# Kernel optimization log

Measured on AMD Instinct MI355X. Metric: run time of the kernel, lower is better.

The kernel has to match this reference:

```python
import jax, jax.numpy as jnp
import numpy as np

N, E, H, ED = 50000, 400000, 512, 64
BN_EPS = 1e-5


def setup_inputs() -> dict:
    key = jax.random.key(0)
    ks = jax.random.split(key, 8)
    s = lambda d: 1.0 / np.sqrt(d)
    return {
        "x": jax.random.normal(ks[0], (N, H), jnp.float32),
        "edge_attr": jax.random.normal(ks[1], (E, ED), jnp.float32),
        "edge_index": jax.random.randint(ks[2], (2, E), 0, N, jnp.int32),
        # GINEConv edge projection (edge_dim -> hidden_dim)
        "W_e": jax.random.normal(ks[3], (ED, H), jnp.float32) * s(ED),
        "b_e": jnp.zeros((H,), jnp.float32),
        # 2-layer MLP: Linear(H, 2H) -> BN -> SiLU -> Linear(2H, H)
        "W1": jax.random.normal(ks[4], (H, 2 * H), jnp.float32) * s(H),
        "b1": jnp.zeros((2 * H,), jnp.float32),
        "g1": jnp.ones((2 * H,), jnp.float32),
        "beta1": jnp.zeros((2 * H,), jnp.float32),
        "W2": jax.random.normal(ks[5], (2 * H, H), jnp.float32) * s(2 * H),
        "b2": jnp.zeros((H,), jnp.float32),
        # outer BatchNorm(hidden_dim)
        "g2": jnp.ones((H,), jnp.float32),
        "beta2": jnp.zeros((H,), jnp.float32),
        # trainable GIN epsilon (init 0)
        "eps": jnp.zeros((), jnp.float32),
    }


def _bn(h, g, b):
    # training-mode batch norm over the node dimension (biased variance)
    mu = jnp.mean(h, axis=0)
    var = jnp.mean(jnp.square(h - mu), axis=0)
    return (h - mu) * jax.lax.rsqrt(var + BN_EPS) * g + b


def reference(x, edge_attr, edge_index, W_e, b_e, W1, b1, g1, beta1, W2, b2, g2, beta2, eps):
    src, dst = edge_index[0], edge_index[1]
    # message: ReLU(x_j + lin(e_ij)), gathered per edge  -> [E, H]
    msg = jax.nn.relu(x[src] + edge_attr @ W_e + b_e)
    # scatter-add aggregate into destination nodes -> [N, H]
    aggr = jax.ops.segment_sum(msg, dst, num_segments=x.shape[0])
    # GIN combine + 2-layer MLP with internal BatchNorm + SiLU (dropout=0)
    h = (1.0 + eps) * x + aggr
    h = jax.nn.silu(_bn(h @ W1 + b1, g1, beta1))
    h = h @ W2 + b2
    # outer BatchNorm + SiLU (dropout=0 -> identity)
    return jax.nn.silu(_bn(h, g2, beta2))
```

## Files before the change

### kernel.cpp

```cpp
#include <hip/hip_runtime.h>
#include <math.h>

#define NN 50000
#define NE 400000
#define HD 512
#define EDIM 64
#define H2 1024
#define LDT 72
#define CAP_SLOT 1200000
#define CAP_TILE 75000
#define CAP_HEAVY 8192
#define NBLK_SCAN 98

typedef short s16x8 __attribute__((ext_vector_type(8)));
typedef float f32x4 __attribute__((ext_vector_type(4)));

__device__ __forceinline__ unsigned short f2bf(float f) {
    union { float f; unsigned u; } v; v.f = f;
    unsigned r = v.u + 0x7fffu + ((v.u >> 16) & 1u);
    return (unsigned short)(r >> 16);
}
__device__ __forceinline__ float bf2f(unsigned short h) {
    union { unsigned u; float f; } v; v.u = ((unsigned)h) << 16;
    return v.f;
}
__device__ __forceinline__ float silu_f(float t) {
    return t / (1.f + __expf(-t));
}
__device__ __forceinline__ void gload_lds16(const unsigned short* g, unsigned short* l) {
    __builtin_amdgcn_global_load_lds(
        (const __attribute__((address_space(1))) unsigned int*)(g),
        (__attribute__((address_space(3))) unsigned int*)(l), 16, 0, 0);
}

constexpr size_t OFF_AGGRC = 0;
constexpr size_t OFF_XB   = 16777216;
constexpr size_t OFF_H1   = 0;
constexpr size_t OFF_H    = 102400000;
constexpr size_t OFF_WET  = 153600000;
constexpr size_t OFF_W1T  = OFF_WET + 65536;
constexpr size_t OFF_W2T  = OFF_W1T + 1048576;
constexpr size_t OFF_CNT  = OFF_W2T + 1048576;
constexpr size_t OFF_B1S  = OFF_CNT + 200000;
constexpr size_t OFF_B1Q  = OFF_B1S + 4096;
constexpr size_t OFF_B2S  = OFF_B1Q + 4096;
constexpr size_t OFF_B2Q  = OFF_B2S + 2048;
constexpr size_t ZERO_BYTES = 200000 + 4096 + 4096 + 2048 + 2048;
constexpr size_t OFF_TEX  = OFF_B2Q + 2048;
constexpr size_t OFF_BSUM = OFF_TEX + 200000;
constexpr size_t OFF_BOFF = OFF_BSUM + 512;
constexpr size_t OFF_T    = OFF_BOFF + 512;
constexpr size_t OFF_CUR  = OFF_T + 64;
constexpr size_t OFF_NOT  = OFF_CUR + 200000;
constexpr size_t OFF_SRCP = OFF_NOT + 300032;
constexpr size_t OFF_EIXP = OFF_SRCP + 4800000;
constexpr size_t OFF_SC1  = OFF_EIXP + 4800000;
constexpr size_t OFF_SB1  = OFF_SC1 + 4096;
constexpr size_t OFF_SC2  = OFF_SB1 + 4096;
constexpr size_t OFF_SB2  = OFF_SC2 + 2048;

__global__ __launch_bounds__(256) void k_convert(const float* __restrict__ We,
    const float* __restrict__ W1, const float* __restrict__ W2,
    unsigned short* __restrict__ wet, unsigned short* __restrict__ w1t,
    unsigned short* __restrict__ w2t) {
    int i = blockIdx.x * 256 + threadIdx.x;
    if (i < 32768) {
        int n = i >> 6, k = i & 63;
        wet[i] = f2bf(We[k * HD + n]);
    } else if (i < 32768 + 524288) {
        int j = i - 32768;
        int n = j >> 9, k = j & 511;
        w1t[j] = f2bf(W1[k * H2 + n]);
    } else if (i < 32768 + 2 * 524288) {
        int j = i - (32768 + 524288);
        int n = j >> 10, k = j & 1023;
        w2t[j] = f2bf(W2[k * HD + n]);
    }
}

__global__ __launch_bounds__(256) void k_xconv(const float* __restrict__ x,
    unsigned short* __restrict__ xb) {
    int t = blockIdx.x * 256 + threadIdx.x;
    if (t >= NN * 64) return;
    int n = t >> 6, rem = t & 63;
    int cb = rem >> 4, l = rem & 15;
    const float* src = x + (size_t)n * HD + cb * 128 + l;
    unsigned short o[8];
    #pragma unroll
    for (int j = 0; j < 8; ++j) o[j] = f2bf(src[j * 16]);
    *(uint4*)(xb + (size_t)n * HD + cb * 128 + l * 8) = *(const uint4*)o;
}

__global__ __launch_bounds__(256) void k_hist(const int* __restrict__ dst, int* __restrict__ counts) {
    int e = blockIdx.x * 256 + threadIdx.x;
    if (e < NE) atomicAdd(&counts[dst[e]], 1);
}

__global__ __launch_bounds__(512) void k_scan1(const int* __restrict__ counts,
    int* __restrict__ tile_excl, int* __restrict__ bsum) {
    __shared__ int wsums[8];
    int b = blockIdx.x, t = threadIdx.x;
    int i = b * 512 + t;
    int c = (i < NN) ? counts[i] : 0;
    int v = 0;
    if (c > 8) v = (c + 15) >> 4;
    else if (c >= 1) v = 0x10000;
    int lane = t & 63, wid = t >> 6;
    int x = v;
    #pragma unroll
    for (int o = 1; o < 64; o <<= 1) {
        int y = __shfl_up(x, o, 64);
        if (lane >= o) x += y;
    }
    if (lane == 63) wsums[wid] = x;
    __syncthreads();
    if (t == 0) {
        int run = 0;
        for (int w = 0; w < 8; ++w) { int tmp = wsums[w]; wsums[w] = run; run += tmp; }
    }
    __syncthreads();
    int excl = x - v + wsums[wid];
    if (i < NN) tile_excl[i] = excl;
    if (t == 511) bsum[b] = excl + v;
}

__global__ void k_scan2(int* __restrict__ bsum, int* __restrict__ boff, int* __restrict__ Tout) {
    if (threadIdx.x == 0) {
        int runf = 0, runh = 0;
        for (int b = 0; b < NBLK_SCAN; ++b) {
            int pk = bsum[b];
            boff[b] = runf;
            bsum[b] = runh;
            runf += pk & 0xFFFF;
            runh += pk >> 16;
        }
        Tout[0] = runf;
        Tout[1] = 0;
        Tout[2] = runh;
    }
}

__global__ __launch_bounds__(512) void k_scan3(const int* __restrict__ counts,
    int* __restrict__ tile_excl, const int* __restrict__ boff, const int* __restrict__ bsum,
    int* __restrict__ cursor, int* __restrict__ node_of_tile, int* __restrict__ Tout) {
    int b = blockIdx.x, t = threadIdx.x;
    int i = b * 512 + t;
    if (i >= NN) return;
    int c = counts[i];
    int pk = tile_excl[i];
    int hid = -1;
    if (c >= 1 && c <= 8) {
        int halfidx = (pk >> 16) + bsum[b];
        int tile = Tout[0] + (halfidx >> 1);
        cursor[i] = tile * 16 + (halfidx & 1) * 8;
        ((unsigned short*)node_of_tile)[tile * 2 + (halfidx & 1)] = (unsigned short)i;
    } else if (c > 8) {
        int tc = (c + 15) >> 4;
        int ts = (pk & 0xFFFF) + boff[b];
        cursor[i] = ts * 16;
        if (c <= 16) {
            node_of_tile[ts] = (int)(0xFFFF0000u | (unsigned)i);
        } else {
            hid = atomicAdd(&Tout[1], 1);
            if (hid >= CAP_HEAVY) hid = CAP_HEAVY - 1;
            for (int k = 0; k < tc; ++k)
                node_of_tile[ts + k] = (int)(0xFFFE0000u | (unsigned)hid);
        }
    }
    tile_excl[i] = hid;
}

__global__ __launch_bounds__(256) void k_scatter(const int* __restrict__ src, const int* __restrict__ dst,
    int* __restrict__ cursor, int* __restrict__ srcp, int* __restrict__ eidxp) {
    int e = blockIdx.x * 256 + threadIdx.x;
    if (e < NE) {
        int d = dst[e];
        int p = atomicAdd(&cursor[d], 1);
        srcp[p] = src[e];
        eidxp[p] = e;
    }
}

__global__ __launch_bounds__(256, 4) void k_edge(
    const float* __restrict__ ea, const unsigned short* __restrict__ wet,
    const unsigned short* __restrict__ xb, const float* __restrict__ b_e,
    const float* __restrict__ eps,
    const int* __restrict__ srcp, const int* __restrict__ eidxp,
    const int* __restrict__ node_of_tile, const int* __restrict__ Tptr,
    float* __restrict__ aggrc, unsigned short* __restrict__ h) {
    int tile0 = blockIdx.x * 2;
    int T = Tptr[0] + ((Tptr[2] + 1) >> 1);
    if (tile0 >= T) return;
    __shared__ unsigned short As[32 * LDT];
    __shared__ int Ss[32];
    __shared__ float Rs[4][256];
    int t = threadIdx.x;
    int slot0 = tile0 * 16;
    {
        int r = t >> 3, qq = t & 7;
        int s = srcp[slot0 + r];
        if (qq == 0) Ss[r] = s;
        unsigned short* lp = As + r * LDT + qq * 8;
        if (s >= 0) {
            int eix = eidxp[slot0 + r];
            const float* gp = ea + (size_t)eix * EDIM + qq * 8;
            float4 v0 = ((const float4*)gp)[0];
            float4 v1 = ((const float4*)gp)[1];
            lp[0] = f2bf(v0.x); lp[1] = f2bf(v0.y); lp[2] = f2bf(v0.z); lp[3] = f2bf(v0.w);
            lp[4] = f2bf(v1.x); lp[5] = f2bf(v1.y); lp[6] = f2bf(v1.z); lp[7] = f2bf(v1.w);
        } else {
            uint4 z = {0u, 0u, 0u, 0u};
            *(uint4*)lp = z;
        }
    }
    __syncthreads();
    int wave = t >> 6, lane = t & 63, l15 = lane & 15, quad = lane >> 4;
    int cblk = wave * 128;
    f32x4 acc[2][8];
    #pragma unroll
    for (int i = 0; i < 2; ++i)
        #pragma unroll
        for (int j = 0; j < 8; ++j) acc[i][j] = (f32x4){0.f, 0.f, 0.f, 0.f};
    #pragma unroll
    for (int k0 = 0; k0 < 64; k0 += 32) {
        s16x8 af[2], bfr[8];
        #pragma unroll
        for (int i = 0; i < 2; ++i)
            af[i] = *(const s16x8*)(As + (i * 16 + l15) * LDT + k0 + quad * 8);
        #pragma unroll
        for (int j = 0; j < 8; ++j)
            bfr[j] = *(const s16x8*)(wet + (size_t)(cblk + j * 16 + l15) * EDIM + k0 + quad * 8);
        #pragma unroll
        for (int i = 0; i < 2; ++i)
            #pragma unroll
            for (int j = 0; j < 8; ++j)
                acc[i][j] = __builtin_amdgcn_mfma_f32_16x16x32_bf16(af[i], bfr[j], acc[i][j], 0, 0, 0);
    }
    float ep = 1.0f + eps[0];
    float bev[8];
    #pragma unroll
    for (int j = 0; j < 8; ++j) bev[j] = b_e[cblk + j * 16 + l15];
    float* rp = Rs[wave];
    #pragma unroll
    for (int i = 0; i < 2; ++i) {
        int tile = tile0 + i;
        unsigned meta = (unsigned)node_of_tile[tile];
        unsigned idA = meta & 0xFFFFu, idB = meta >> 16;
        bool pair = idB < 0xFFFEu;
        int v_own = pair ? (quad < 2 ? (int)idA : (int)idB) : (int)idA;
        int vc = v_own < NN ? v_own : 0;
        int srow = i * 16 + quad * 4;
        s16x8 xr[4]; float msk[4];
        #pragma unroll
        for (int r = 0; r < 4; ++r) {
            int s = Ss[srow + r];
            msk[r] = s >= 0 ? 1.f : 0.f;
            xr[r] = *(const s16x8*)(xb + (size_t)(s >= 0 ? s : 0) * HD + cblk + l15 * 8);
        }
        s16x8 xo = *(const s16x8*)(xb + (size_t)vc * HD + cblk + l15 * 8);
        float sum8[8];
        #pragma unroll
        for (int j = 0; j < 8; ++j) sum8[j] = 0.f;
        #pragma unroll
        for (int r = 0; r < 4; ++r) {
            #pragma unroll
            for (int j = 0; j < 8; ++j) {
                float vv = acc[i][j][r] + bf2f((unsigned short)xr[r][j]) + bev[j];
                vv = vv > 0.f ? vv : 0.f;
                sum8[j] = fmaf(msk[r], vv, sum8[j]);
            }
        }
        #pragma unroll
        for (int j = 0; j < 8; ++j) sum8[j] += __shfl_xor(sum8[j], 16, 64);
        if (tile < T) {
            if (pair) {
                #pragma unroll
                for (int j = 0; j < 8; ++j) {
                    float val = fmaf(ep, bf2f((unsigned short)xo[j]), sum8[j]);
                    if (quad == 0) rp[j * 16 + l15] = val;
                    if (quad == 2) rp[128 + j * 16 + l15] = val;
                }
                __builtin_amdgcn_sched_barrier(0);
                int l2 = lane & 31;
                const float* rb_ = rp + (lane >> 5) * 128 + l2 * 4;
                float4 v4 = *(const float4*)rb_;
                uint2 pk;
                pk.x = (unsigned)f2bf(v4.x) | ((unsigned)f2bf(v4.y) << 16);
                pk.y = (unsigned)f2bf(v4.z) | ((unsigned)f2bf(v4.w) << 16);
                *(uint2*)(h + (size_t)v_own * HD + cblk + l2 * 4) = pk;
            } else {
                #pragma unroll
                for (int j = 0; j < 8; ++j) sum8[j] += __shfl_xor(sum8[j], 32, 64);
                if (idB == 0xFFFEu) {
                    if (quad == 0) {
                        float* ap = aggrc + (size_t)idA * HD + cblk;
                        #pragma unroll
                        for (int j = 0; j < 8; ++j) atomicAdd(ap + j * 16 + l15, sum8[j]);
                    }
                } else {
                    int j0 = quad * 2, j1 = j0 + 1;
                    rp[j0 * 16 + l15] = fmaf(ep, bf2f((unsigned short)xo[j0]), sum8[j0]);
                    rp[j1 * 16 + l15] = fmaf(ep, bf2f((unsigned short)xo[j1]), sum8[j1]);
                    __builtin_amdgcn_sched_barrier(0);
                    unsigned pk = (unsigned)f2bf(rp[lane * 2]) |
                                  ((unsigned)f2bf(rp[lane * 2 + 1]) << 16);
                    *(unsigned*)(h + (size_t)idA * HD + cblk + lane * 2) = pk;
                }
            }
        }
    }
}

__global__ __launch_bounds__(256) void k_combine_heavy(const float* __restrict__ aggrc,
    const float* __restrict__ x, const int* __restrict__ counts, const int* __restrict__ hidmap,
    const float* __restrict__ eps, unsigned short* __restrict__ h) {
    long i = ((long)blockIdx.x * 256 + threadIdx.x) * 4;
    if (i >= (long)NN * HD) return;
    int v = (int)(i >> 9);
    int c = counts[v];
    if (c >= 1 && c <= 16) return;
    float ep = 1.0f + eps[0];
    float4 a = {0.f, 0.f, 0.f, 0.f};
    if (c > 16) a = *(const float4*)(aggrc + (size_t)hidmap[v] * HD + (i & (HD - 1)));
    float4 xv = *(const float4*)(x + i);
    uint2 p;
    p.x = (unsigned)f2bf(ep * xv.x + a.x) | ((unsigned)f2bf(ep * xv.y + a.y) << 16);
    p.y = (unsigned)f2bf(ep * xv.z + a.z) | ((unsigned)f2bf(ep * xv.w + a.w) << 16);
    *(uint2*)(h + i) = p;
}

template <bool BF16OUT, bool SILU_A>
__global__ __launch_bounds__(256) void k_gemm_bn(
    const unsigned short* __restrict__ A, const unsigned short* __restrict__ Bt,
    const float* __restrict__ bias, void* __restrict__ Cv,
    float* __restrict__ bn_sum, float* __restrict__ bn_sumsq,
    const float* __restrict__ a_sc, const float* __restrict__ a_sb,
    int M, int K, int Nn) {
    __shared__ unsigned short As[SILU_A ? (64 * LDT) : (64 * 64)];
    __shared__ unsigned short Bs[128 * 64];
    __shared__ float csum[128], csumsq[128];
    constexpr int LDA = SILU_A ? LDT : 64;
    int nwg = gridDim.x;
    int q = nwg >> 3, r = nwg & 7;
    int xk = blockIdx.x & 7, xj = blockIdx.x >> 3;
    int logical = xk * q + (xk < r ? xk : r) + xj;
    int nnb = Nn >> 7;
    int mblk = logical / nnb, nblk = logical - mblk * nnb;
    int t = threadIdx.x;
    int row0 = mblk * 64, col0 = nblk * 128;
    int wid = t >> 6, lane = t & 63, l15 = lane & 15, quad = lane >> 4;
    int wr = wid >> 1, wc = wid & 1;
    int rb = (lane >> 3), cb8 = (lane & 7) * 8;
    int scb8 = cb8 ^ (rb * 8);
    int rswz = (l15 & 7) * 8;
    f32x4 acc[2][4];
    #pragma unroll
    for (int i = 0; i < 2; ++i)
        #pragma unroll
        for (int j = 0; j < 4; ++j) acc[i][j] = (f32x4){0.f, 0.f, 0.f, 0.f};

    for (int k0 = 0; k0 < K; k0 += 64) {
        __syncthreads();
        #pragma unroll
        for (int c = 0; c < 4; ++c) {
            int row = (wid * 4 + c) * 8 + rb;
            gload_lds16(Bt + (size_t)(col0 + row) * K + k0 + scb8,
                        Bs + row * 64 + cb8);
        }
        if constexpr (!SILU_A) {
            #pragma unroll
            for (int c = 0; c < 2; ++c) {
                int row = (wid * 2 + c) * 8 + rb;
                gload_lds16(A + (size_t)(row0 + row) * K + k0 + scb8,
                            As + row * 64 + cb8);
            }
        } else {
            int rr = t >> 2, qtr = t & 3;
            int row = row0 + rr;
            int kb = k0 + qtr * 16;
            unsigned short* lp = As + rr * LDT + qtr * 16;
            if (row < M) {
                const unsigned short* gp = A + (size_t)row * K + kb;
                #pragma unroll
                for (int jj = 0; jj < 2; ++jj) {
                    uint4 u = *(const uint4*)(gp + jj * 8);
                    float4 sA = *(const float4*)(a_sc + kb + jj * 8);
                    float4 sB = *(const float4*)(a_sc + kb + jj * 8 + 4);
                    float4 bA = *(const float4*)(a_sb + kb + jj * 8);
                    float4 bB = *(const float4*)(a_sb + kb + jj * 8 + 4);
                    unsigned short o[8];
                    o[0] = f2bf(silu_f(bf2f((unsigned short)(u.x & 0xffffu)) * sA.x + bA.x));
                    o[1] = f2bf(silu_f(bf2f((unsigned short)(u.x >> 16)) * sA.y + bA.y));
                    o[2] = f2bf(silu_f(bf2f((unsigned short)(u.y & 0xffffu)) * sA.z + bA.z));
                    o[3] = f2bf(silu_f(bf2f((unsigned short)(u.y >> 16)) * sA.w + bA.w));
                    o[4] = f2bf(silu_f(bf2f((unsigned short)(u.z & 0xffffu)) * sB.x + bB.x));
                    o[5] = f2bf(silu_f(bf2f((unsigned short)(u.z >> 16)) * sB.y + bB.y));
                    o[6] = f2bf(silu_f(bf2f((unsigned short)(u.w & 0xffffu)) * sB.z + bB.z));
                    o[7] = f2bf(silu_f(bf2f((unsigned short)(u.w >> 16)) * sB.w + bB.w));
                    #pragma unroll
                    for (int m = 0; m < 8; ++m) lp[jj * 8 + m] = o[m];
                }
            } else {
                uint4 z = {0u, 0u, 0u, 0u};
                *(uint4*)(lp) = z;
                *(uint4*)(lp + 8) = z;
            }
        }
        __syncthreads();
        #pragma unroll
        for (int kk = 0; kk < 64; kk += 32) {
            s16x8 af[2], bfr[4];
            #pragma unroll
            for (int i = 0; i < 2; ++i) {
                if constexpr (SILU_A)
                    af[i] = *(const s16x8*)(As + (wr * 32 + i * 16 + l15) * LDA + kk + quad * 8);
                else
                    af[i] = *(const s16x8*)(As + (wr * 32 + i * 16 + l15) * 64 + ((kk + quad * 8) ^ rswz));
            }
            #pragma unroll
            for (int j = 0; j < 4; ++j)
                bfr[j] = *(const s16x8*)(Bs + (wc * 64 + j * 16 + l15) * 64 + ((kk + quad * 8) ^ rswz));
            #pragma unroll
            for (int i = 0; i < 2; ++i)
                #pragma unroll
                for (int j = 0; j < 4; ++j)
                    acc[i][j] = __builtin_amdgcn_mfma_f32_16x16x32_bf16(af[i], bfr[j], acc[i][j], 0, 0, 0);
        }
    }
    if (t < 128) { csum[t] = 0.f; csumsq[t] = 0.f; }
    __syncthreads();
    int mrow0 = row0 + wr * 32;
    #pragma unroll
    for (int j = 0; j < 4; ++j) {
        int col = wc * 64 + j * 16 + l15;
        float bv = bias[col0 + col];
        float ls = 0.f, lq = 0.f;
        #pragma unroll
        for (int i = 0; i < 2; ++i) {
            #pragma unroll
            for (int r2 = 0; r2 < 4; ++r2) {
                int row = mrow0 + i * 16 + quad * 4 + r2;
                if (row < M) {
                    float v = acc[i][j][r2] + bv;
                    if (BF16OUT)
                        ((unsigned short*)Cv)[(size_t)row * Nn + col0 + col] = f2bf(v);
                    else
                        ((float*)Cv)[(size_t)row * Nn + col0 + col] = v;
                    ls += v; lq += v * v;
                }
            }
        }
        ls += __shfl_xor(ls, 16, 64); ls += __shfl_xor(ls, 32, 64);
        lq += __shfl_xor(lq, 16, 64); lq += __shfl_xor(lq, 32, 64);
        if (quad == 0) {
            atomicAdd(&csum[col], ls);
            atomicAdd(&csumsq[col], lq);
        }
    }
    __syncthreads();
    if (t < 128) {
        atomicAdd(bn_sum + col0 + t, csum[t]);
        atomicAdd(bn_sumsq + col0 + t, csumsq[t]);
    }
}

__global__ __launch_bounds__(256) void k_bn_final(const float* __restrict__ s,
    const float* __restrict__ q, const float* __restrict__ g, const float* __restrict__ beta,
    float* __restrict__ scale, float* __restrict__ sbias, int C, float invN) {
    int c = blockIdx.x * 256 + threadIdx.x;
    if (c < C) {
        float mu = s[c] * invN;
        float var = q[c] * invN - mu * mu;
        var = fmaxf(var, 0.f);
        float sc = g[c] * rsqrtf(var + 1e-5f);
        scale[c] = sc;
        sbias[c] = beta[c] - mu * sc;
    }
}

__global__ __launch_bounds__(256) void k_out(float* __restrict__ out,
    const float* __restrict__ sc, const float* __restrict__ sb, long total) {
    long i = ((long)blockIdx.x * 256 + threadIdx.x) * 4;
    if (i >= total) return;
    int c = (int)(i & (HD - 1));
    float4 v = *(const float4*)(out + i);
    float4 s4 = *(const float4*)(sc + c);
    float4 b4 = *(const float4*)(sb + c);
    float4 o;
    o.x = silu_f(v.x * s4.x + b4.x);
    o.y = silu_f(v.y * s4.y + b4.y);
    o.z = silu_f(v.z * s4.z + b4.z);
    o.w = silu_f(v.w * s4.w + b4.w);
    *(float4*)(out + i) = o;
}

extern "C" void kernel_launch(void* const* d_in, const int* in_sizes, int n_in,
                              void* d_out, int out_size, void* d_ws, size_t ws_size,
                              hipStream_t stream) {
    const float* x      = (const float*)d_in[0];
    const float* ea     = (const float*)d_in[1];
    const int*   ei     = (const int*)d_in[2];
    const float* W_e    = (const float*)d_in[3];
    const float* b_e    = (const float*)d_in[4];
    const float* W1     = (const float*)d_in[5];
    const float* b1     = (const float*)d_in[6];
    const float* g1     = (const float*)d_in[7];
    const float* beta1  = (const float*)d_in[8];
    const float* W2     = (const float*)d_in[9];
    const float* b2     = (const float*)d_in[10];
    const float* g2     = (const float*)d_in[11];
    const float* beta2  = (const float*)d_in[12];
    const float* eps    = (const float*)d_in[13];
    float* out = (float*)d_out;
    char* ws = (char*)d_ws;

    float*          aggrc = (float*)(ws + OFF_AGGRC);
    unsigned short* xb   = (unsigned short*)(ws + OFF_XB);
    unsigned short* h1   = (unsigned short*)(ws + OFF_H1);
    unsigned short* h    = (unsigned short*)(ws + OFF_H);
    unsigned short* wet  = (unsigned short*)(ws + OFF_WET);
    unsigned short* w1t  = (unsigned short*)(ws + OFF_W1T);
    unsigned short* w2t  = (unsigned short*)(ws + OFF_W2T);
    int* counts  = (int*)(ws + OFF_CNT);
    float* b1s   = (float*)(ws + OFF_B1S);
    float* b1q   = (float*)(ws + OFF_B1Q);
    float* b2s   = (float*)(ws + OFF_B2S);
    float* b2q   = (float*)(ws + OFF_B2Q);
    int* tex     = (int*)(ws + OFF_TEX);
    int* bsum    = (int*)(ws + OFF_BSUM);
    int* boff    = (int*)(ws + OFF_BOFF);
    int* Tptr    = (int*)(ws + OFF_T);
    int* cursor  = (int*)(ws + OFF_CUR);
    int* notile  = (int*)(ws + OFF_NOT);
    int* srcp    = (int*)(ws + OFF_SRCP);
    int* eidxp   = (int*)(ws + OFF_EIXP);
    float* sc1   = (float*)(ws + OFF_SC1);
    float* sb1   = (float*)(ws + OFF_SB1);
    float* sc2   = (float*)(ws + OFF_SC2);
    float* sb2   = (float*)(ws + OFF_SB2);

    hipMemsetAsync(aggrc, 0, (size_t)CAP_HEAVY * HD * 4, stream);
    hipMemsetAsync(ws + OFF_CNT, 0, ZERO_BYTES, stream);
    hipMemsetAsync(notile, 0xFF, 300032, stream);
    hipMemsetAsync(srcp, 0xFF, (size_t)CAP_SLOT * 4, stream);
    k_convert<<<4224, 256, 0, stream>>>(W_e, W1, W2, wet, w1t, w2t);
    k_xconv<<<(NN * 64 + 255) / 256, 256, 0, stream>>>(x, xb);
    k_hist<<<(NE + 255) / 256, 256, 0, stream>>>(ei + NE, counts);
    k_scan1<<<NBLK_SCAN, 512, 0, stream>>>(counts, tex, bsum);
    k_scan2<<<1, 64, 0, stream>>>(bsum, boff, Tptr);
    k_scan3<<<NBLK_SCAN, 512, 0, stream>>>(counts, tex, boff, bsum, cursor, notile, Tptr);
    k_scatter<<<(NE + 255) / 256, 256, 0, stream>>>(ei, ei + NE, cursor, srcp, eidxp);
    k_edge<<<CAP_TILE / 2, 256, 0, stream>>>(ea, wet, xb, b_e, eps, srcp, eidxp, notile, Tptr, aggrc, h);
    k_combine_heavy<<<(int)(((long)NN * HD / 4 + 255) / 256), 256, 0, stream>>>(
        aggrc, x, counts, tex, eps, h);
    k_gemm_bn<true, false><<<((NN + 63) / 64) * (H2 / 128), 256, 0, stream>>>(
        h, w1t, b1, h1, b1s, b1q, nullptr, nullptr, NN, HD, H2);
    k_bn_final<<<4, 256, 0, stream>>>(b1s, b1q, g1, beta1, sc1, sb1, H2, 1.f / NN);
    k_gemm_bn<false, true><<<((NN + 63) / 64) * (HD / 128), 256, 0, stream>>>(
        h1, w2t, b2, out, b2s, b2q, sc1, sb1, NN, H2, HD);
    k_bn_final<<<2, 256, 0, stream>>>(b2s, b2q, g2, beta2, sc2, sb2, HD, 1.f / NN);
    k_out<<<(int)(((long)NN * HD / 4 + 255) / 256), 256, 0, stream>>>(out, sc2, sb2, (long)NN * HD);
}
```

Baseline: 836.2 us.

## Double-buffer LDS tiles in GEMM+BN kernel to overlap loads with MFMA

Splits the A and B shared-memory tiles into two buffers and prefetches the next K-step's tiles (async global-to-LDS for B and plain A, register prefetch for the SiLU-transformed A) while MFMAs run on the current buffer. One barrier per K-step replaces two. This is meant to hide global-load latency behind compute, at the cost of doubled LDS use and more registers, which can lower occupancy.

```diff
diff --git a/kernel.cpp b/kernel.cpp
--- a/kernel.cpp
+++ b/kernel.cpp
@@ -336,8 +336,8 @@
     float* __restrict__ bn_sum, float* __restrict__ bn_sumsq,
     const float* __restrict__ a_sc, const float* __restrict__ a_sb,
     int M, int K, int Nn) {
-    __shared__ unsigned short As[SILU_A ? (64 * LDT) : (64 * 64)];
-    __shared__ unsigned short Bs[128 * 64];
+    __shared__ unsigned short As[2][SILU_A ? (64 * LDT) : (64 * 64)];
+    __shared__ unsigned short Bs[2][128 * 64];
     __shared__ float csum[128], csumsq[128];
     constexpr int LDA = SILU_A ? LDT : 64;
     int nwg = gridDim.x;
@@ -353,80 +353,109 @@
     int rb = (lane >> 3), cb8 = (lane & 7) * 8;
     int scb8 = cb8 ^ (rb * 8);
     int rswz = (l15 & 7) * 8;
+    int rr = t >> 2, qtr = t & 3;
+    int arow = row0 + rr;
     f32x4 acc[2][4];
     #pragma unroll
     for (int i = 0; i < 2; ++i)
         #pragma unroll
         for (int j = 0; j < 4; ++j) acc[i][j] = (f32x4){0.f, 0.f, 0.f, 0.f};
 
-    for (int k0 = 0; k0 < K; k0 += 64) {
-        __syncthreads();
+    auto stageB = [&](int buf, int k0) {
         #pragma unroll
         for (int c = 0; c < 4; ++c) {
             int row = (wid * 4 + c) * 8 + rb;
             gload_lds16(Bt + (size_t)(col0 + row) * K + k0 + scb8,
-                        Bs + row * 64 + cb8);
-        }
-        if constexpr (!SILU_A) {
-            #pragma unroll
-            for (int c = 0; c < 2; ++c) {
-                int row = (wid * 2 + c) * 8 + rb;
-                gload_lds16(A + (size_t)(row0 + row) * K + k0 + scb8,
-                            As + row * 64 + cb8);
-            }
-        } else {
-            int rr = t >> 2, qtr = t & 3;
-            int row = row0 + rr;
-            int kb = k0 + qtr * 16;
-            unsigned short* lp = As + rr * LDT + qtr * 16;
-            if (row < M) {
-                const unsigned short* gp = A + (size_t)row * K + kb;
-                #pragma unroll
-                for (int jj = 0; jj < 2; ++jj) {
-                    uint4 u = *(const uint4*)(gp + jj * 8);
-                    float4 sA = *(const float4*)(a_sc + kb + jj * 8);
-                    float4 sB = *(const float4*)(a_sc + kb + jj * 8 + 4);
-                    float4 bA = *(const float4*)(a_sb + kb + jj * 8);
-                    float4 bB = *(const float4*)(a_sb + kb + jj * 8 + 4);
-                    unsigned short o[8];
-                    o[0] = f2bf(silu_f(bf2f((unsigned short)(u.x & 0xffffu)) * sA.x + bA.x));
-                    o[1] = f2bf(silu_f(bf2f((unsigned short)(u.x >> 16)) * sA.y + bA.y));
-                    o[2] = f2bf(silu_f(bf2f((unsigned short)(u.y & 0xffffu)) * sA.z + bA.z));
-                    o[3] = f2bf(silu_f(bf2f((unsigned short)(u.y >> 16)) * sA.w + bA.w));
-                    o[4] = f2bf(silu_f(bf2f((unsigned short)(u.z & 0xffffu)) * sB.x + bB.x));
-                    o[5] = f2bf(silu_f(bf2f((unsigned short)(u.z >> 16)) * sB.y + bB.y));
-                    o[6] = f2bf(silu_f(bf2f((unsigned short)(u.w & 0xffffu)) * sB.z + bB.z));
-                    o[7] = f2bf(silu_f(bf2f((unsigned short)(u.w >> 16)) * sB.w + bB.w));
-                    #pragma unroll
-                    for (int m = 0; m < 8; ++m) lp[jj * 8 + m] = o[m];
-                }
-            } else {
-                uint4 z = {0u, 0u, 0u, 0u};
-                *(uint4*)(lp) = z;
-                *(uint4*)(lp + 8) = z;
-            }
-        }
-        __syncthreads();
+                        Bs[buf] + row * 64 + cb8);
+        }
+    };
+    auto stageA_g = [&](int buf, int k0) {
+        #pragma unroll
+        for (int c = 0; c < 2; ++c) {
+            int row = (wid * 2 + c) * 8 + rb;
+            gload_lds16(A + (size_t)(row0 + row) * K + k0 + scb8,
+                        As[buf] + row * 64 + cb8);
+        }
+    };
+    auto loadA_regs = [&](int k0, uint4* au) {
+        const unsigned short* gp = A + (size_t)arow * K + k0 + qtr * 16;
+        #pragma unroll
+        for (int jj = 0; jj < 2; ++jj) {
+            uint4 z = {0u, 0u, 0u, 0u};
+            au[jj] = (arow < M) ? *(const uint4*)(gp + jj * 8) : z;
+        }
+    };
+    auto writeA_silu = [&](int buf, int k0, const uint4* au) {
+        int kb = k0 + qtr * 16;
+        unsigned short* lp = As[buf] + rr * LDT + qtr * 16;
+        #pragma unroll
+        for (int jj = 0; jj < 2; ++jj) {
+            uint4 u = au[jj];
+            float4 sA = *(const float4*)(a_sc + kb + jj * 8);
+            float4 sB = *(const float4*)(a_sc + kb + jj * 8 + 4);
+            float4 bA = *(const float4*)(a_sb + kb + jj * 8);
+            float4 bB = *(const float4*)(a_sb + kb + jj * 8 + 4);
+            unsigned short o[8];
+            o[0] = f2bf(silu_f(bf2f((unsigned short)(u.x & 0xffffu)) * sA.x + bA.x));
+            o[1] = f2bf(silu_f(bf2f((unsigned short)(u.x >> 16)) * sA.y + bA.y));
+            o[2] = f2bf(silu_f(bf2f((unsigned short)(u.y & 0xffffu)) * sA.z + bA.z));
+            o[3] = f2bf(silu_f(bf2f((unsigned short)(u.y >> 16)) * sA.w + bA.w));
+            o[4] = f2bf(silu_f(bf2f((unsigned short)(u.z & 0xffffu)) * sB.x + bB.x));
+            o[5] = f2bf(silu_f(bf2f((unsigned short)(u.z >> 16)) * sB.y + bB.y));
+            o[6] = f2bf(silu_f(bf2f((unsigned short)(u.w & 0xffffu)) * sB.z + bB.z));
+            o[7] = f2bf(silu_f(bf2f((unsigned short)(u.w >> 16)) * sB.w + bB.w));
+            #pragma unroll
+            for (int m = 0; m < 8; ++m) lp[jj * 8 + m] = o[m];
+        }
+    };
+
+    stageB(0, 0);
+    if constexpr (!SILU_A) {
+        stageA_g(0, 0);
+    } else {
+        uint4 au0[2];
+        loadA_regs(0, au0);
+        writeA_silu(0, 0, au0);
+    }
+    __syncthreads();
+
+    int nsteps = K >> 6;
+    int cur = 0;
+    for (int s = 0; s < nsteps; ++s) {
+        bool hn = (s + 1) < nsteps;
+        int k0n = (s + 1) << 6;
+        uint4 au[2];
+        if (hn) {
+            stageB(cur ^ 1, k0n);
+            if constexpr (!SILU_A) stageA_g(cur ^ 1, k0n);
+            else loadA_regs(k0n, au);
+        }
         #pragma unroll
         for (int kk = 0; kk < 64; kk += 32) {
             s16x8 af[2], bfr[4];
             #pragma unroll
             for (int i = 0; i < 2; ++i) {
                 if constexpr (SILU_A)
-                    af[i] = *(const s16x8*)(As + (wr * 32 + i * 16 + l15) * LDA + kk + quad * 8);
+                    af[i] = *(const s16x8*)(As[cur] + (wr * 32 + i * 16 + l15) * LDA + kk + quad * 8);
                 else
-                    af[i] = *(const s16x8*)(As + (wr * 32 + i * 16 + l15) * 64 + ((kk + quad * 8) ^ rswz));
+                    af[i] = *(const s16x8*)(As[cur] + (wr * 32 + i * 16 + l15) * 64 + ((kk + quad * 8) ^ rswz));
             }
             #pragma unroll
             for (int j = 0; j < 4; ++j)
-                bfr[j] = *(const s16x8*)(Bs + (wc * 64 + j * 16 + l15) * 64 + ((kk + quad * 8) ^ rswz));
+                bfr[j] = *(const s16x8*)(Bs[cur] + (wc * 64 + j * 16 + l15) * 64 + ((kk + quad * 8) ^ rswz));
             #pragma unroll
             for (int i = 0; i < 2; ++i)
                 #pragma unroll
                 for (int j = 0; j < 4; ++j)
                     acc[i][j] = __builtin_amdgcn_mfma_f32_16x16x32_bf16(af[i], bfr[j], acc[i][j], 0, 0, 0);
         }
-    }
+        if (hn) {
+            if constexpr (SILU_A) writeA_silu(cur ^ 1, k0n, au);
+        }
+        __syncthreads();
+        cur ^= 1;
+    }
+
     if (t < 128) { csum[t] = 0.f; csumsq[t] = 0.f; }
     __syncthreads();
     int mrow0 = row0 + wr * 32;
```

New measurement: 1.012 ms. +21.0%, slower.
